# Performance work log

Hardware: AMD Instinct MI355X
Metric: run time of the kernel (lower is better)

The kernel has to match this reference:

```python
import jax, jax.numpy as jnp
import numpy as np

N, H, W, C = 2048, 64, 64, 8
E, G, M = 4, 512, 512            # experts, group size per class, max_output_cells
CELLS = [128, 256, 384, 512]     # classes_config.values()


def setup_inputs() -> dict:
    key = jax.random.key(0)
    k = jax.random.split(key, 6)
    inputs = jax.random.normal(k[0], (N, H, W, C), dtype=jnp.float32)
    # input_config: class -> sample indices (equal partition of the batch)
    indices = jnp.arange(N, dtype=jnp.int32).reshape(E, G)
    W1 = jax.random.normal(k[1], (E, 1, 1, C, C), dtype=jnp.float32) * 0.1
    W3 = jax.random.normal(k[2], (E, 3, 3, C, C), dtype=jnp.float32) * 0.1
    Wskip = jax.random.normal(k[3], (E, 1, 1, C, 2 * C), dtype=jnp.float32) * 0.1
    Wd = jax.random.normal(k[4], (E, 2 * C, M), dtype=jnp.float32) * 0.1
    # zero-pad each expert's output beyond its num_output_layer_cells
    cell_mask = (jnp.arange(M)[None, :] < jnp.asarray(CELLS)[:, None]).astype(jnp.float32)
    return {"inputs": inputs, "indices": indices, "W1": W1, "W3": W3,
            "Wskip": Wskip, "Wd": Wd, "cell_mask": cell_mask}


def _conv(x, w):
    # x: [G,H,W,Cin], w: [kh,kw,Cin,Cout] -> [G,H,W,Cout], SAME padding
    return jax.lax.conv_general_dilated(x, w, (1, 1), 'SAME',
                                        dimension_numbers=('NHWC', 'HWIO', 'NHWC'))


def _expert(x, w1, w3, ws, wd, mask):
    # Hybrid inception + skip: parallel 1x1/3x3 branches, channel concat, 1x1-projected skip
    b1 = jax.nn.relu(_conv(x, w1))           # [G,H,W,C]
    b2 = jax.nn.relu(_conv(x, w3))           # [G,H,W,C]
    y = jnp.concatenate([b1, b2], axis=-1) + _conv(x, ws)  # [G,H,W,2C]
    pooled = y.mean(axis=(1, 2))             # [G,2C]
    return (pooled @ wd) * mask[None, :]     # [G,M], padded to max_output_cells


def reference(inputs, indices, W1, W3, Wskip, Wd, cell_mask):
    # class-indexed gather: [E,G,H,W,C]
    groups = inputs[indices]
    # dispatch each group to its expert, vmapped over experts
    outs = jax.vmap(_expert)(groups, W1, W3, Wskip, Wd, cell_mask)  # [E,G,M]
    # concat along batch in class order (matches outputs.extend + tf.concat axis=0)
    return outs.reshape(E * G, M)
```

## Files before the change

### kernel.cpp

```cpp
#include <hip/hip_runtime.h>
#include <hip/hip_bf16.h>

#define MM 512
#define ROWSZ (66 * 8)

typedef short bf16x8 __attribute__((ext_vector_type(8)));
typedef float f32x4  __attribute__((ext_vector_type(4)));

static __device__ inline short f2bf(float f) {
    __hip_bfloat16 h = __float2bfloat16(f);
    return *reinterpret_cast<short*>(&h);
}

__global__ __launch_bounds__(256, 4)
void conv_moe_mfma(const float* __restrict__ x,
                   const int*   __restrict__ idx,
                   const float* __restrict__ W1,
                   const float* __restrict__ W3,
                   const float* __restrict__ Wsk,
                   const float* __restrict__ Wd,
                   const float* __restrict__ cmask,
                   float*       __restrict__ out)
{
    __shared__ short xbf[2][18][66][8];
    __shared__ float red[4][16];
    __shared__ float redx[4][8];
    __shared__ float rsum[16];
    __shared__ float rsumx[8];
    __shared__ float pooledS[16];

    const int b    = blockIdx.x;
    const int e    = b >> 9;
    const int tid  = threadIdx.x;
    const int lane = tid & 63;
    const int wid  = tid >> 6;
    const int g    = lane >> 4;
    const int p    = lane & 15;
    const int CB   = wid << 4;

    const int samp = idx[b];
    const float* xb = x + (size_t)samp * 32768;

    const float* w3 = W3 + e * 576;
    const float* w1 = W1 + e * 64;
    bf16x8 B0, B1, B2;
    #pragma unroll
    for (int j = 0; j < 8; ++j) {
        float v0 = 0.f, v1 = 0.f, v2 = 0.f;
        if (g < 3) {
            if (p >= 8) {
                v0 = w3[(0 * 3 + g) * 64 + j * 8 + (p - 8)];
                v1 = w3[(1 * 3 + g) * 64 + j * 8 + (p - 8)];
                v2 = w3[(2 * 3 + g) * 64 + j * 8 + (p - 8)];
            } else if (g == 1) {
                v1 = w1[j * 8 + p];
            }
        }
        B0[j] = f2bf(v0); B1[j] = f2bf(v1); B2[j] = f2bf(v2);
    }

    const int gi  = (g < 3) ? g : 2;
    const int offA = (CB + p + gi) * 8;

    if (tid < 144) {
        const int bb = tid & 1, t = tid >> 1;
        const int rr = t >> 1, side = t & 1;
        if (rr < 18) {
            bf16x8 zv = {0,0,0,0,0,0,0,0};
            *(bf16x8*)&xbf[bb][rr][side ? 65 : 0][0] = zv;
        }
    }

    const float4 z4 = make_float4(0.f, 0.f, 0.f, 0.f);
    float4 ra[5][2];
    float4 sxa = z4, sxb = z4;

    #pragma unroll
    for (int j5 = 0; j5 < 5; ++j5) {
        const int j = j5 * 256 + tid;
        ra[j5][0] = z4; ra[j5][1] = z4;
        if (j < 1152) {
            const int lrow = j >> 6, c = j & 63;
            const int r = lrow - 1;
            if (r >= 0) {
                const float4* s4 = (const float4*)(xb + (((r << 6) + c) << 3));
                ra[j5][0] = s4[0];
                ra[j5][1] = s4[1];
            }
        }
    }
    #pragma unroll
    for (int j5 = 0; j5 < 5; ++j5) {
        const int j = j5 * 256 + tid;
        if (j < 1152) {
            const int lrow = j >> 6, c = j & 63;
            sxa.x += ra[j5][0].x; sxa.y += ra[j5][0].y;
            sxa.z += ra[j5][0].z; sxa.w += ra[j5][0].w;
            sxb.x += ra[j5][1].x; sxb.y += ra[j5][1].y;
            sxb.z += ra[j5][1].z; sxb.w += ra[j5][1].w;
            bf16x8 v;
            v[0] = f2bf(ra[j5][0].x); v[1] = f2bf(ra[j5][0].y);
            v[2] = f2bf(ra[j5][0].z); v[3] = f2bf(ra[j5][0].w);
            v[4] = f2bf(ra[j5][1].x); v[5] = f2bf(ra[j5][1].y);
            v[6] = f2bf(ra[j5][1].z); v[7] = f2bf(ra[j5][1].w);
            *(bf16x8*)&xbf[0][lrow][c + 1][0] = v;
        }
    }
    __syncthreads();

    f32x4 ssum = {0.f, 0.f, 0.f, 0.f};

    #pragma unroll 1
    for (int s = 0; s < 4; ++s) {
        if (s < 3) {
            const int rbase = 16 * (s + 1) + 1;
            #pragma unroll
            for (int j5 = 0; j5 < 4; ++j5) {
                const int j = j5 * 256 + tid;
                const int lrow = j >> 6, c = j & 63;
                const int r = rbase + lrow;
                ra[j5][0] = z4; ra[j5][1] = z4;
                if (r < 64) {
                    const float4* s4 = (const float4*)(xb + (((r << 6) + c) << 3));
                    ra[j5][0] = s4[0];
                    ra[j5][1] = s4[1];
                }
            }
        }

        {
            const short* base = &xbf[s & 1][0][0][0] + offA;
            bf16x8 A0 = *(const bf16x8*)(base + 0 * ROWSZ);
            bf16x8 A1 = *(const bf16x8*)(base + 1 * ROWSZ);
            bf16x8 A2 = *(const bf16x8*)(base + 2 * ROWSZ);
            #pragma unroll 3
            for (int rl = 0; rl < 15; ++rl) {
                const bf16x8 A3 = *(const bf16x8*)(base + (rl + 3) * ROWSZ);
                f32x4 d = {0.f, 0.f, 0.f, 0.f};
                d = __builtin_amdgcn_mfma_f32_16x16x32_bf16(A0, B0, d, 0, 0, 0);
                d = __builtin_amdgcn_mfma_f32_16x16x32_bf16(A1, B1, d, 0, 0, 0);
                d = __builtin_amdgcn_mfma_f32_16x16x32_bf16(A2, B2, d, 0, 0, 0);
                ssum[0] += fmaxf(d[0], 0.f);
                ssum[1] += fmaxf(d[1], 0.f);
                ssum[2] += fmaxf(d[2], 0.f);
                ssum[3] += fmaxf(d[3], 0.f);
                A0 = A1; A1 = A2; A2 = A3;
            }
            f32x4 d = {0.f, 0.f, 0.f, 0.f};
            d = __builtin_amdgcn_mfma_f32_16x16x32_bf16(A0, B0, d, 0, 0, 0);
            d = __builtin_amdgcn_mfma_f32_16x16x32_bf16(A1, B1, d, 0, 0, 0);
            d = __builtin_amdgcn_mfma_f32_16x16x32_bf16(A2, B2, d, 0, 0, 0);
            ssum[0] += fmaxf(d[0], 0.f);
            ssum[1] += fmaxf(d[1], 0.f);
            ssum[2] += fmaxf(d[2], 0.f);
            ssum[3] += fmaxf(d[3], 0.f);
        }

        if (s < 3) {
            const int bn = (s + 1) & 1;
            if (tid < 128) {
                const bf16x8 rcopy =
                    *(const bf16x8*)&xbf[s & 1][16 + (tid >> 6)][(tid & 63) + 1][0];
                *(bf16x8*)&xbf[bn][tid >> 6][(tid & 63) + 1][0] = rcopy;
            }
            #pragma unroll
            for (int j5 = 0; j5 < 4; ++j5) {
                const int j = j5 * 256 + tid;
                const int lrow = 2 + (j >> 6), c = j & 63;
                sxa.x += ra[j5][0].x; sxa.y += ra[j5][0].y;
                sxa.z += ra[j5][0].z; sxa.w += ra[j5][0].w;
                sxb.x += ra[j5][1].x; sxb.y += ra[j5][1].y;
                sxb.z += ra[j5][1].z; sxb.w += ra[j5][1].w;
                bf16x8 v;
                v[0] = f2bf(ra[j5][0].x); v[1] = f2bf(ra[j5][0].y);
                v[2] = f2bf(ra[j5][0].z); v[3] = f2bf(ra[j5][0].w);
                v[4] = f2bf(ra[j5][1].x); v[5] = f2bf(ra[j5][1].y);
                v[6] = f2bf(ra[j5][1].z); v[7] = f2bf(ra[j5][1].w);
                *(bf16x8*)&xbf[bn][lrow][c + 1][0] = v;
            }
            __syncthreads();
        }
    }

    float scon = ssum[0] + ssum[1] + ssum[2] + ssum[3];
    scon += __shfl_xor(scon, 16);
    scon += __shfl_xor(scon, 32);
    if (lane < 16) red[wid][lane] = scon;

    float sxv[8] = {sxa.x, sxa.y, sxa.z, sxa.w, sxb.x, sxb.y, sxb.z, sxb.w};
    #pragma unroll
    for (int i = 0; i < 8; ++i)
        #pragma unroll
        for (int off = 32; off > 0; off >>= 1)
            sxv[i] += __shfl_xor(sxv[i], off);
    if (lane == 0)
        #pragma unroll
        for (int i = 0; i < 8; ++i) redx[wid][i] = sxv[i];
    __syncthreads();

    if (tid < 16) rsum[tid]  = (red[0][tid] + red[1][tid] + red[2][tid] + red[3][tid]) * (1.f / 4096.f);
    if (tid < 8)  rsumx[tid] = (redx[0][tid] + redx[1][tid] + redx[2][tid] + redx[3][tid]) * (1.f / 4096.f);
    __syncthreads();

    if (tid < 16) {
        float acc = rsum[tid];
        #pragma unroll
        for (int ci = 0; ci < 8; ++ci)
            acc += rsumx[ci] * Wsk[e * 128 + ci * 16 + tid];
        pooledS[tid] = acc;
    }
    __syncthreads();

    const float* wd = Wd + (size_t)e * 16 * MM;
    const float* cm = cmask + e * MM;
    #pragma unroll 1
    for (int m = tid; m < MM; m += 256) {
        float acc = 0.f;
        #pragma unroll
        for (int k = 0; k < 16; ++k) acc += pooledS[k] * wd[k * MM + m];
        out[(size_t)b * MM + m] = acc * cm[m];
    }
}

extern "C" void kernel_launch(void* const* d_in, const int* in_sizes, int n_in,
                              void* d_out, int out_size, void* d_ws, size_t ws_size,
                              hipStream_t stream) {
    const float* x    = (const float*)d_in[0];
    const int*   idx  = (const int*)  d_in[1];
    const float* W1   = (const float*)d_in[2];
    const float* W3   = (const float*)d_in[3];
    const float* Wsk  = (const float*)d_in[4];
    const float* Wd   = (const float*)d_in[5];
    const float* cmsk = (const float*)d_in[6];
    float* out = (float*)d_out;

    conv_moe_mfma<<<2048, 256, 0, stream>>>(x, idx, W1, W3, Wsk, Wd, cmsk, out);
}
```

Baseline: 49.77 us.

## Process two samples per block and prefetch next sample during last stage

The grid is halved so each block handles two samples (b and b+1024). During the final row-stage of the first sample, it loads the first 18 rows of the second sample into registers, which hides that sample's initial load latency. The tradeoff is fewer blocks in flight and a longer serial chain per block. The edge-zeroing was also narrowed to 72 threads, the exact count that is needed.

Result: slower. 61.61 us (+23.8%).

```diff
diff --git a/kernel.cpp b/kernel.cpp
--- a/kernel.cpp
+++ b/kernel.cpp
@@ -29,8 +29,6 @@
     __shared__ float rsumx[8];
     __shared__ float pooledS[16];
 
-    const int b    = blockIdx.x;
-    const int e    = b >> 9;
     const int tid  = threadIdx.x;
     const int lane = tid & 63;
     const int wid  = tid >> 6;
@@ -38,135 +36,41 @@
     const int p    = lane & 15;
     const int CB   = wid << 4;
 
-    const int samp = idx[b];
-    const float* xb = x + (size_t)samp * 32768;
-
-    const float* w3 = W3 + e * 576;
-    const float* w1 = W1 + e * 64;
-    bf16x8 B0, B1, B2;
-    #pragma unroll
-    for (int j = 0; j < 8; ++j) {
-        float v0 = 0.f, v1 = 0.f, v2 = 0.f;
-        if (g < 3) {
-            if (p >= 8) {
-                v0 = w3[(0 * 3 + g) * 64 + j * 8 + (p - 8)];
-                v1 = w3[(1 * 3 + g) * 64 + j * 8 + (p - 8)];
-                v2 = w3[(2 * 3 + g) * 64 + j * 8 + (p - 8)];
-            } else if (g == 1) {
-                v1 = w1[j * 8 + p];
-            }
-        }
-        B0[j] = f2bf(v0); B1[j] = f2bf(v1); B2[j] = f2bf(v2);
-    }
-
-    const int gi  = (g < 3) ? g : 2;
+    const int gi   = (g < 3) ? g : 2;
     const int offA = (CB + p + gi) * 8;
 
-    if (tid < 144) {
+    if (tid < 72) {
         const int bb = tid & 1, t = tid >> 1;
         const int rr = t >> 1, side = t & 1;
-        if (rr < 18) {
-            bf16x8 zv = {0,0,0,0,0,0,0,0};
-            *(bf16x8*)&xbf[bb][rr][side ? 65 : 0][0] = zv;
-        }
+        bf16x8 zv = {0,0,0,0,0,0,0,0};
+        *(bf16x8*)&xbf[bb][rr][side ? 65 : 0][0] = zv;
     }
 
     const float4 z4 = make_float4(0.f, 0.f, 0.f, 0.f);
     float4 ra[5][2];
     float4 sxa = z4, sxb = z4;
 
-    #pragma unroll
-    for (int j5 = 0; j5 < 5; ++j5) {
-        const int j = j5 * 256 + tid;
-        ra[j5][0] = z4; ra[j5][1] = z4;
-        if (j < 1152) {
-            const int lrow = j >> 6, c = j & 63;
-            const int r = lrow - 1;
-            if (r >= 0) {
-                const float4* s4 = (const float4*)(xb + (((r << 6) + c) << 3));
-                ra[j5][0] = s4[0];
-                ra[j5][1] = s4[1];
-            }
-        }
-    }
-    #pragma unroll
-    for (int j5 = 0; j5 < 5; ++j5) {
-        const int j = j5 * 256 + tid;
-        if (j < 1152) {
-            const int lrow = j >> 6, c = j & 63;
-            sxa.x += ra[j5][0].x; sxa.y += ra[j5][0].y;
-            sxa.z += ra[j5][0].z; sxa.w += ra[j5][0].w;
-            sxb.x += ra[j5][1].x; sxb.y += ra[j5][1].y;
-            sxb.z += ra[j5][1].z; sxb.w += ra[j5][1].w;
-            bf16x8 v;
-            v[0] = f2bf(ra[j5][0].x); v[1] = f2bf(ra[j5][0].y);
-            v[2] = f2bf(ra[j5][0].z); v[3] = f2bf(ra[j5][0].w);
-            v[4] = f2bf(ra[j5][1].x); v[5] = f2bf(ra[j5][1].y);
-            v[6] = f2bf(ra[j5][1].z); v[7] = f2bf(ra[j5][1].w);
-            *(bf16x8*)&xbf[0][lrow][c + 1][0] = v;
-        }
-    }
-    __syncthreads();
-
-    f32x4 ssum = {0.f, 0.f, 0.f, 0.f};
-
-    #pragma unroll 1
-    for (int s = 0; s < 4; ++s) {
-        if (s < 3) {
-            const int rbase = 16 * (s + 1) + 1;
-            #pragma unroll
-            for (int j5 = 0; j5 < 4; ++j5) {
-                const int j = j5 * 256 + tid;
+    {
+        const float* xb0 = x + (size_t)idx[blockIdx.x] * 32768;
+        #pragma unroll
+        for (int j5 = 0; j5 < 5; ++j5) {
+            const int j = j5 * 256 + tid;
+            ra[j5][0] = z4; ra[j5][1] = z4;
+            if (j < 1152) {
                 const int lrow = j >> 6, c = j & 63;
-                const int r = rbase + lrow;
-                ra[j5][0] = z4; ra[j5][1] = z4;
-                if (r < 64) {
-                    const float4* s4 = (const float4*)(xb + (((r << 6) + c) << 3));
+                const int r = lrow - 1;
+                if (r >= 0) {
+                    const float4* s4 = (const float4*)(xb0 + (((r << 6) + c) << 3));
                     ra[j5][0] = s4[0];
                     ra[j5][1] = s4[1];
                 }
             }
         }
-
-        {
-            const short* base = &xbf[s & 1][0][0][0] + offA;
-            bf16x8 A0 = *(const bf16x8*)(base + 0 * ROWSZ);
-            bf16x8 A1 = *(const bf16x8*)(base + 1 * ROWSZ);
-            bf16x8 A2 = *(const bf16x8*)(base + 2 * ROWSZ);
-            #pragma unroll 3
-            for (int rl = 0; rl < 15; ++rl) {
-                const bf16x8 A3 = *(const bf16x8*)(base + (rl + 3) * ROWSZ);
-                f32x4 d = {0.f, 0.f, 0.f, 0.f};
-                d = __builtin_amdgcn_mfma_f32_16x16x32_bf16(A0, B0, d, 0, 0, 0);
-                d = __builtin_amdgcn_mfma_f32_16x16x32_bf16(A1, B1, d, 0, 0, 0);
-                d = __builtin_amdgcn_mfma_f32_16x16x32_bf16(A2, B2, d, 0, 0, 0);
-                ssum[0] += fmaxf(d[0], 0.f);
-                ssum[1] += fmaxf(d[1], 0.f);
-                ssum[2] += fmaxf(d[2], 0.f);
-                ssum[3] += fmaxf(d[3], 0.f);
-                A0 = A1; A1 = A2; A2 = A3;
-            }
-            f32x4 d = {0.f, 0.f, 0.f, 0.f};
-            d = __builtin_amdgcn_mfma_f32_16x16x32_bf16(A0, B0, d, 0, 0, 0);
-            d = __builtin_amdgcn_mfma_f32_16x16x32_bf16(A1, B1, d, 0, 0, 0);
-            d = __builtin_amdgcn_mfma_f32_16x16x32_bf16(A2, B2, d, 0, 0, 0);
-            ssum[0] += fmaxf(d[0], 0.f);
-            ssum[1] += fmaxf(d[1], 0.f);
-            ssum[2] += fmaxf(d[2], 0.f);
-            ssum[3] += fmaxf(d[3], 0.f);
-        }
-
-        if (s < 3) {
-            const int bn = (s + 1) & 1;
-            if (tid < 128) {
-                const bf16x8 rcopy =
-                    *(const bf16x8*)&xbf[s & 1][16 + (tid >> 6)][(tid & 63) + 1][0];
-                *(bf16x8*)&xbf[bn][tid >> 6][(tid & 63) + 1][0] = rcopy;
-            }
-            #pragma unroll
-            for (int j5 = 0; j5 < 4; ++j5) {
-                const int j = j5 * 256 + tid;
-                const int lrow = 2 + (j >> 6), c = j & 63;
+        #pragma unroll
+        for (int j5 = 0; j5 < 5; ++j5) {
+            const int j = j5 * 256 + tid;
+            if (j < 1152) {
+                const int lrow = j >> 6, c = j & 63;
                 sxa.x += ra[j5][0].x; sxa.y += ra[j5][0].y;
                 sxa.z += ra[j5][0].z; sxa.w += ra[j5][0].w;
                 sxb.x += ra[j5][1].x; sxb.y += ra[j5][1].y;
@@ -176,49 +80,186 @@
                 v[2] = f2bf(ra[j5][0].z); v[3] = f2bf(ra[j5][0].w);
                 v[4] = f2bf(ra[j5][1].x); v[5] = f2bf(ra[j5][1].y);
                 v[6] = f2bf(ra[j5][1].z); v[7] = f2bf(ra[j5][1].w);
-                *(bf16x8*)&xbf[bn][lrow][c + 1][0] = v;
-            }
-            __syncthreads();
-        }
-    }
-
-    float scon = ssum[0] + ssum[1] + ssum[2] + ssum[3];
-    scon += __shfl_xor(scon, 16);
-    scon += __shfl_xor(scon, 32);
-    if (lane < 16) red[wid][lane] = scon;
-
-    float sxv[8] = {sxa.x, sxa.y, sxa.z, sxa.w, sxb.x, sxb.y, sxb.z, sxb.w};
-    #pragma unroll
-    for (int i = 0; i < 8; ++i)
-        #pragma unroll
-        for (int off = 32; off > 0; off >>= 1)
-            sxv[i] += __shfl_xor(sxv[i], off);
-    if (lane == 0)
-        #pragma unroll
-        for (int i = 0; i < 8; ++i) redx[wid][i] = sxv[i];
-    __syncthreads();
-
-    if (tid < 16) rsum[tid]  = (red[0][tid] + red[1][tid] + red[2][tid] + red[3][tid]) * (1.f / 4096.f);
-    if (tid < 8)  rsumx[tid] = (redx[0][tid] + redx[1][tid] + redx[2][tid] + redx[3][tid]) * (1.f / 4096.f);
-    __syncthreads();
-
-    if (tid < 16) {
-        float acc = rsum[tid];
-        #pragma unroll
-        for (int ci = 0; ci < 8; ++ci)
-            acc += rsumx[ci] * Wsk[e * 128 + ci * 16 + tid];
-        pooledS[tid] = acc;
+                *(bf16x8*)&xbf[0][lrow][c + 1][0] = v;
+            }
+        }
     }
     __syncthreads();
 
-    const float* wd = Wd + (size_t)e * 16 * MM;
-    const float* cm = cmask + e * MM;
     #pragma unroll 1
-    for (int m = tid; m < MM; m += 256) {
-        float acc = 0.f;
-        #pragma unroll
-        for (int k = 0; k < 16; ++k) acc += pooledS[k] * wd[k * MM + m];
-        out[(size_t)b * MM + m] = acc * cm[m];
+    for (int q = 0; q < 2; ++q) {
+        const int b = blockIdx.x + (q << 10);
+        const int e = b >> 9;
+        const float* xb = x + (size_t)idx[b] * 32768;
+
+        const float* w3 = W3 + e * 576;
+        const float* w1 = W1 + e * 64;
+        bf16x8 B0, B1, B2;
+        #pragma unroll
+        for (int j = 0; j < 8; ++j) {
+            float v0 = 0.f, v1 = 0.f, v2 = 0.f;
+            if (g < 3) {
+                if (p >= 8) {
+                    v0 = w3[(0 * 3 + g) * 64 + j * 8 + (p - 8)];
+                    v1 = w3[(1 * 3 + g) * 64 + j * 8 + (p - 8)];
+                    v2 = w3[(2 * 3 + g) * 64 + j * 8 + (p - 8)];
+                } else if (g == 1) {
+                    v1 = w1[j * 8 + p];
+                }
+            }
+            B0[j] = f2bf(v0); B1[j] = f2bf(v1); B2[j] = f2bf(v2);
+        }
+
+        f32x4 ssum = {0.f, 0.f, 0.f, 0.f};
+
+        #pragma unroll 1
+        for (int s = 0; s < 4; ++s) {
+            if (s < 3) {
+                const int rbase = 16 * (s + 1) + 1;
+                #pragma unroll
+                for (int j5 = 0; j5 < 4; ++j5) {
+                    const int j = j5 * 256 + tid;
+                    const int lrow = j >> 6, c = j & 63;
+                    const int r = rbase + lrow;
+                    ra[j5][0] = z4; ra[j5][1] = z4;
+                    if (r < 64) {
+                        const float4* s4 = (const float4*)(xb + (((r << 6) + c) << 3));
+                        ra[j5][0] = s4[0];
+                        ra[j5][1] = s4[1];
+                    }
+                }
+            } else if (q == 0) {
+                const float* xbn = x + (size_t)idx[blockIdx.x + 1024] * 32768;
+                #pragma unroll
+                for (int j5 = 0; j5 < 5; ++j5) {
+                    const int j = j5 * 256 + tid;
+                    ra[j5][0] = z4; ra[j5][1] = z4;
+                    if (j < 1152) {
+                        const int lrow = j >> 6, c = j & 63;
+                        const int r = lrow - 1;
+                        if (r >= 0) {
+                            const float4* s4 = (const float4*)(xbn + (((r << 6) + c) << 3));
+                            ra[j5][0] = s4[0];
+                            ra[j5][1] = s4[1];
+                        }
+                    }
+                }
+            }
+
+            {
+                const short* base = &xbf[s & 1][0][0][0] + offA;
+                bf16x8 A0 = *(const bf16x8*)(base + 0 * ROWSZ);
+                bf16x8 A1 = *(const bf16x8*)(base + 1 * ROWSZ);
+                bf16x8 A2 = *(const bf16x8*)(base + 2 * ROWSZ);
+                #pragma unroll 3
+                for (int rl = 0; rl < 15; ++rl) {
+                    const bf16x8 A3 = *(const bf16x8*)(base + (rl + 3) * ROWSZ);
+                    f32x4 d = {0.f, 0.f, 0.f, 0.f};
+                    d = __builtin_amdgcn_mfma_f32_16x16x32_bf16(A0, B0, d, 0, 0, 0);
+                    d = __builtin_amdgcn_mfma_f32_16x16x32_bf16(A1, B1, d, 0, 0, 0);
+                    d = __builtin_amdgcn_mfma_f32_16x16x32_bf16(A2, B2, d, 0, 0, 0);
+                    ssum[0] += fmaxf(d[0], 0.f);
+                    ssum[1] += fmaxf(d[1], 0.f);
+                    ssum[2] += fmaxf(d[2], 0.f);
+                    ssum[3] += fmaxf(d[3], 0.f);
+                    A0 = A1; A1 = A2; A2 = A3;
+                }
+                f32x4 d = {0.f, 0.f, 0.f, 0.f};
+                d = __builtin_amdgcn_mfma_f32_16x16x32_bf16(A0, B0, d, 0, 0, 0);
+                d = __builtin_amdgcn_mfma_f32_16x16x32_bf16(A1, B1, d, 0, 0, 0);
+                d = __builtin_amdgcn_mfma_f32_16x16x32_bf16(A2, B2, d, 0, 0, 0);
+                ssum[0] += fmaxf(d[0], 0.f);
+                ssum[1] += fmaxf(d[1], 0.f);
+                ssum[2] += fmaxf(d[2], 0.f);
+                ssum[3] += fmaxf(d[3], 0.f);
+            }
+
+            if (s < 3) {
+                const int bn = (s + 1) & 1;
+                if (tid < 128) {
+                    const bf16x8 rcopy =
+                        *(const bf16x8*)&xbf[s & 1][16 + (tid >> 6)][(tid & 63) + 1][0];
+                    *(bf16x8*)&xbf[bn][tid >> 6][(tid & 63) + 1][0] = rcopy;
+                }
+                #pragma unroll
+                for (int j5 = 0; j5 < 4; ++j5) {
+                    const int j = j5 * 256 + tid;
+                    const int lrow = 2 + (j >> 6), c = j & 63;
+                    sxa.x += ra[j5][0].x; sxa.y += ra[j5][0].y;
+                    sxa.z += ra[j5][0].z; sxa.w += ra[j5][0].w;
+                    sxb.x += ra[j5][1].x; sxb.y += ra[j5][1].y;
+                    sxb.z += ra[j5][1].z; sxb.w += ra[j5][1].w;
+                    bf16x8 v;
+                    v[0] = f2bf(ra[j5][0].x); v[1] = f2bf(ra[j5][0].y);
+                    v[2] = f2bf(ra[j5][0].z); v[3] = f2bf(ra[j5][0].w);
+                    v[4] = f2bf(ra[j5][1].x); v[5] = f2bf(ra[j5][1].y);
+                    v[6] = f2bf(ra[j5][1].z); v[7] = f2bf(ra[j5][1].w);
+                    *(bf16x8*)&xbf[bn][lrow][c + 1][0] = v;
+                }
+                __syncthreads();
+            }
+        }
+
+        float scon = ssum[0] + ssum[1] + ssum[2] + ssum[3];
+        scon += __shfl_xor(scon, 16);
+        scon += __shfl_xor(scon, 32);
+        if (lane < 16) red[wid][lane] = scon;
+
+        float sxv[8] = {sxa.x, sxa.y, sxa.z, sxa.w, sxb.x, sxb.y, sxb.z, sxb.w};
+        #pragma unroll
+        for (int i = 0; i < 8; ++i)
+            #pragma unroll
+            for (int off = 32; off > 0; off >>= 1)
+                sxv[i] += __shfl_xor(sxv[i], off);
+        if (lane == 0)
+            #pragma unroll
+            for (int i = 0; i < 8; ++i) redx[wid][i] = sxv[i];
+        __syncthreads();
+
+        if (tid < 16) rsum[tid]  = (red[0][tid] + red[1][tid] + red[2][tid] + red[3][tid]) * (1.f / 4096.f);
+        if (tid < 8)  rsumx[tid] = (redx[0][tid] + redx[1][tid] + redx[2][tid] + redx[3][tid]) * (1.f / 4096.f);
+        __syncthreads();
+
+        if (tid < 16) {
+            float acc = rsum[tid];
+            #pragma unroll
+            for (int ci = 0; ci < 8; ++ci)
+                acc += rsumx[ci] * Wsk[e * 128 + ci * 16 + tid];
+            pooledS[tid] = acc;
+        }
+        __syncthreads();
+
+        const float* wd = Wd + (size_t)e * 16 * MM;
+        const float* cm = cmask + e * MM;
+        #pragma unroll 1
+        for (int m = tid; m < MM; m += 256) {
+            float acc = 0.f;
+            #pragma unroll
+            for (int k = 0; k < 16; ++k) acc += pooledS[k] * wd[k * MM + m];
+            out[(size_t)b * MM + m] = acc * cm[m];
+        }
+
+        if (q == 0) {
+            sxa = z4; sxb = z4;
+            #pragma unroll
+            for (int j5 = 0; j5 < 5; ++j5) {
+                const int j = j5 * 256 + tid;
+                if (j < 1152) {
+                    const int lrow = j >> 6, c = j & 63;
+                    sxa.x += ra[j5][0].x; sxa.y += ra[j5][0].y;
+                    sxa.z += ra[j5][0].z; sxa.w += ra[j5][0].w;
+                    sxb.x += ra[j5][1].x; sxb.y += ra[j5][1].y;
+                    sxb.z += ra[j5][1].z; sxb.w += ra[j5][1].w;
+                    bf16x8 v;
+                    v[0] = f2bf(ra[j5][0].x); v[1] = f2bf(ra[j5][0].y);
+                    v[2] = f2bf(ra[j5][0].z); v[3] = f2bf(ra[j5][0].w);
+                    v[4] = f2bf(ra[j5][1].x); v[5] = f2bf(ra[j5][1].y);
+                    v[6] = f2bf(ra[j5][1].z); v[7] = f2bf(ra[j5][1].w);
+                    *(bf16x8*)&xbf[0][lrow][c + 1][0] = v;
+                }
+            }
+            __syncthreads();
+        }
     }
 }
 
@@ -234,5 +275,5 @@
     const float* cmsk = (const float*)d_in[6];
     float* out = (float*)d_out;
 
-    conv_moe_mfma<<<2048, 256, 0, stream>>>(x, idx, W1, W3, Wsk, Wd, cmsk, out);
+    conv_moe_mfma<<<1024, 256, 0, stream>>>(x, idx, W1, W3, Wsk, Wd, cmsk, out);
 }
```
